# Kernel optimization log

Measured on AMD Instinct MI355X. Metric: run time of the kernel, lower is better.

Reference implementation:

```python
import jax, jax.numpy as jnp
import numpy as np

# dims / hyperparams (match init_kwargs)
B, C, H, W = 1, 48, 160, 160
COUT = 48
RANK = 12
K = 8          # topK neighbors
WS = 32        # window_size
KS = 3         # local conv kernel / local mask size
M = 3          # circ_rows
DELTA = 10.0
LEAK = 0.01


def circ_dense(x, w, m):
    """CircDense: x (N, Cin), w (Cout//m, 1, Cin) -> (N, Cout).
    Equivalent to circular-pad + conv1d in the torch module."""
    cin = x.shape[1]
    xp = jnp.concatenate([x, x[:, : m - 1]], axis=1)            # circular pad to Cin+m-1
    xw = jnp.stack([xp[:, j : j + cin] for j in range(m)], 1)   # (N, m, Cin)
    out = jnp.einsum('njc,ic->nij', xw, w[:, 0, :])             # (N, Cout//m, m)
    return out.reshape(x.shape[0], -1)


def windowed_topk(h, k, ws, ks):
    """knn.windowedTopK: per 32x32 window, K nearest neighbors by feature L2,
    excluding the ks x ks local neighborhood (localMask). Returns (B,K,H,W)
    global flat pixel indices."""
    b, c, hh, ww = h.shape
    nh, nw = hh // ws, ww // ws
    ws2 = ws * ws
    hw = h.reshape(b, c, nh, ws, nw, ws).transpose(0, 2, 4, 3, 5, 1)
    hw = hw.reshape(b, nh, nw, ws2, c)                          # windowed features
    sq = jnp.sum(hw * hw, -1)
    d = sq[..., :, None] + sq[..., None, :] - 2.0 * jnp.einsum('bijnc,bijmc->bijnm', hw, hw)
    r = jnp.arange(ws2) // ws
    cc = jnp.arange(ws2) % ws
    loc = (jnp.abs(r[:, None] - r[None, :]) <= ks // 2) & (jnp.abs(cc[:, None] - cc[None, :]) <= ks // 2)
    d = jnp.where(loc, 1e10, d)                                 # mask local neighborhood
    _, idx = jax.lax.top_k(-d, k)                               # (b,nh,nw,ws2,k) local idx
    wi = jnp.arange(nh)[:, None, None, None]
    wj = jnp.arange(nw)[None, :, None, None]
    g = (wi * ws + idx // ws) * ww + (wj * ws + idx % ws)       # global flat idx
    g = g.reshape(b, nh, nw, ws, ws, k).transpose(0, 5, 1, 3, 2, 4).reshape(b, k, hh, ww)
    return g


def low_rank_ecc(h, edge, W0, b0, WL, WR, Wk, bk):
    b, k, hh, ww = edge.shape
    n = hh * ww
    cin = h.shape[1]
    hf = h.reshape(b, cin, n)
    ef = edge.reshape(b, k, n)
    # gather neighbor (vertex) features: (b, cin, k, n) -> (b, k, n, cin)
    vertex = jax.vmap(lambda hb, eb: hb[:, eb])(hf, ef).transpose(0, 2, 3, 1)
    center = hf.transpose(0, 2, 1)[:, None]                     # (b,1,n,cin)
    label = vertex - center                                     # edge labels
    lt = label.reshape(-1, cin)                                 # (B0, Cin), B0=b*k*n
    vt = vertex.reshape(-1, cin)
    theta = jax.nn.leaky_relu(lt @ W0.T + b0, LEAK)
    tL = circ_dense(theta, WL, M).reshape(-1, COUT, RANK)       # (B0, Cout, rank)
    tR = circ_dense(theta, WR, M).reshape(-1, cin, RANK)        # (B0, Cin, rank)
    kap = theta @ Wk.T + bk                                     # (B0, rank)
    tmp = kap * jnp.einsum('bcr,bc->br', tR, vt)                # thetaR^T @ v, scaled
    out = jnp.einsum('bor,br->bo', tL, tmp)                     # thetaL @ (...)
    gamma = jnp.exp(-jnp.sum(lt * lt, 1, keepdims=True) / DELTA)
    out = (gamma * out).reshape(b, k, n, COUT).mean(1)          # mean over K neighbors
    return out.transpose(0, 2, 1).reshape(b, COUT, hh, ww)


def local_conv(h, w):
    p = KS // 2
    hp = jnp.pad(h, ((0, 0), (0, 0), (p, p), (p, p)), mode='reflect')
    return jax.lax.conv_general_dilated(hp, w, (1, 1), 'VALID',
                                        dimension_numbers=('NCHW', 'OIHW', 'NCHW'))


def setup_inputs() -> dict:
    key = jax.random.key(0)
    ks_ = jax.random.split(key, 9)
    s_in = 1.0 / np.sqrt(C)
    return {
        'h': jax.random.normal(ks_[0], (B, C, H, W), jnp.float32),
        'W0': jax.random.normal(ks_[1], (C, C), jnp.float32) * s_in,
        'b0': jnp.zeros((C,), jnp.float32),
        'WL': jax.random.normal(ks_[2], (RANK * COUT // M, 1, C), jnp.float32) * s_in,
        'WR': jax.random.normal(ks_[3], (RANK * C // M, 1, C), jnp.float32) * s_in,
        'Wk': jax.random.normal(ks_[4], (RANK, C), jnp.float32) * s_in,
        'bk': jnp.zeros((RANK,), jnp.float32),
        'Wconv': jax.random.normal(ks_[5], (COUT, C, KS, KS), jnp.float32) * (1.0 / np.sqrt(C * KS * KS)),
        'bias': jnp.zeros((1, COUT, 1, 1), jnp.float32),
    }


def reference(h, W0, b0, WL, WR, Wk, bk, Wconv, bias):
    edge = windowed_topk(h, K, WS, KS)
    hNL = low_rank_ecc(h, edge, W0, b0, WL, WR, Wk, bk)
    hL = local_conv(h, Wconv)
    return (hNL + hL) / 2.0 + bias
```

## Files before the change

kernel.cpp:

```cpp
#include <hip/hip_runtime.h>

#define CC    48
#define HH    160
#define WWID  160
#define NPIX  25600
#define KK    8

typedef unsigned short u16;
typedef unsigned int u32;
typedef __attribute__((ext_vector_type(8))) short bf16x8;
typedef __attribute__((ext_vector_type(4))) float f32x4;

__device__ __forceinline__ float bf2f(u16 u) {
    return __uint_as_float(((unsigned int)u) << 16);
}
__device__ __forceinline__ u16 f2bf(float f) {
    unsigned int x = __float_as_uint(f);
    return (u16)((x + 0x7FFFu + ((x >> 16) & 1u)) >> 16);
}

#define OFF_B0    0
#define OFF_BK    48
#define OFF_WKT   60
#define OFF_WBH   636
#define OFF_WBL   8828
#define OFF_WLH   17020
#define OFF_WLL   21628
#define OFF_SQP   26236
#define OFF_W0V   51836
#define OFF_VTB   1280636
#define OFF_HHT   3738236
#define OFF_HLT   4557436
#define OFF_PARTK 5376636
#define OFF_UBAR  7015036

__global__ void prep_kernel(const float* W0, const float* b0, const float* WL,
                            const float* WR, const float* Wk, const float* bk,
                            float* ws) {
    float* b0f = ws + OFF_B0;
    float* bkf = ws + OFF_BK;
    float* wkt = ws + OFF_WKT;
    u16*   wbh = (u16*)(ws + OFF_WBH);
    u16*   wbl = (u16*)(ws + OFF_WBL);
    u16*   wlh = (u16*)(ws + OFF_WLH);
    u16*   wll = (u16*)(ws + OFF_WLL);
    int t = blockIdx.x * 256 + threadIdx.x;
    int stride = gridDim.x * 256;
    for (int i = t; i < 16384; i += stride) {
        int col = i >> 6, k = i & 63;
        float v = 0.f;
        if (k < 48) {
            if (col < 192)      v = WR[(4*k + (col & 3))*48 + (col >> 2)];
            else if (col < 240) v = W0[(col - 192)*48 + k];
        }
        u16 hi = f2bf(v);
        wbh[i] = hi;
        wbl[i] = f2bf(v - bf2f(hi));
    }
    for (int i = t; i < 9216; i += stride) {
        int o = i / 192, k = i % 192;
        float v = WL[(4*o + (k & 3))*48 + (k >> 2)];
        u16 hi = f2bf(v);
        wlh[i] = hi;
        wll[i] = f2bf(v - bf2f(hi));
    }
    for (int i = t; i < 576; i += stride) { int c = i / 12, r = i % 12; wkt[i] = Wk[r*48 + c]; }
    for (int i = t; i < 48; i += stride) { b0f[i] = b0[i]; }
    for (int i = t; i < 12; i += stride) { bkf[i] = bk[i]; }
}

__global__ __launch_bounds__(256) void split_kernel(const float* h, float* sqp,
                                                    u16* hht, u16* hlt) {
    int p = blockIdx.x * 256 + threadIdx.x;
    float sq = 0.f;
    u16 hh[64], hl[64];
    #pragma unroll
    for (int c = 0; c < 48; c++) {
        float v = h[c*NPIX + p];
        sq = fmaf(v, v, sq);
        u16 hi = f2bf(v);
        hh[c] = hi;
        hl[c] = f2bf(v - bf2f(hi));
    }
    #pragma unroll
    for (int c = 48; c < 64; c++) { hh[c] = 0; hl[c] = 0; }
    sqp[p] = sq;
    uint4* dh = (uint4*)&hht[(long)p*64];
    uint4* dl = (uint4*)&hlt[(long)p*64];
    const uint4* s1 = (const uint4*)hh;
    const uint4* s2 = (const uint4*)hl;
    #pragma unroll
    for (int i = 0; i < 8; i++) { dh[i] = s1[i]; dl[i] = s2[i]; }
}

__global__ __launch_bounds__(512) void pixvt_mfma(const u16* hht, const u16* hlt,
                                                  const float* ws, float* w0v, u16* vtb) {
    __shared__ __align__(16) char smem[38912];
    u16*   a_hi = (u16*)smem;
    u16*   a_lo = (u16*)(smem + 8192);
    u16*   vt_s = (u16*)smem;
    float* w0_s = (float*)(smem + 25600);

    const u16* wbh = (const u16*)(ws + OFF_WBH);
    const u16* wbl = (const u16*)(ws + OFF_WBL);

    int tid = threadIdx.x;
    int pbase = blockIdx.x * 64;

    {
        int blk = tid >> 6, row = tid & 63;
        int swz = (blk ^ (row & 7)) * 8;
        *(uint4*)&a_hi[row*64 + swz] = *(const uint4*)&hht[(long)(pbase + row)*64 + blk*8];
        *(uint4*)&a_lo[row*64 + swz] = *(const uint4*)&hlt[(long)(pbase + row)*64 + blk*8];
    }
    __syncthreads();

    int w = tid >> 6, lane = tid & 63;
    int lm = lane & 15, lg = lane >> 4;
    int c2a = 2*w, c2b = 2*w + 1;

    f32x4 acc0[4], acc1[4];
    #pragma unroll
    for (int t = 0; t < 4; t++) { acc0[t] = (f32x4){0.f,0.f,0.f,0.f}; acc1[t] = (f32x4){0.f,0.f,0.f,0.f}; }

    #pragma unroll
    for (int s = 0; s < 2; s++) {
        int lblk = 4*s + lg;
        int aswz = (lblk ^ (lm & 7)) * 8;
        bf16x8 ah0 = *(const bf16x8*)&a_hi[( 0 + lm)*64 + aswz];
        bf16x8 ah1 = *(const bf16x8*)&a_hi[(16 + lm)*64 + aswz];
        bf16x8 ah2 = *(const bf16x8*)&a_hi[(32 + lm)*64 + aswz];
        bf16x8 ah3 = *(const bf16x8*)&a_hi[(48 + lm)*64 + aswz];
        bf16x8 al0 = *(const bf16x8*)&a_lo[( 0 + lm)*64 + aswz];
        bf16x8 al1 = *(const bf16x8*)&a_lo[(16 + lm)*64 + aswz];
        bf16x8 al2 = *(const bf16x8*)&a_lo[(32 + lm)*64 + aswz];
        bf16x8 al3 = *(const bf16x8*)&a_lo[(48 + lm)*64 + aswz];
        {
            int col = c2a*16 + lm;
            bf16x8 bh = *(const bf16x8*)&wbh[col*64 + lblk*8];
            bf16x8 bl = *(const bf16x8*)&wbl[col*64 + lblk*8];
            acc0[0] = __builtin_amdgcn_mfma_f32_16x16x32_bf16(ah0, bh, acc0[0], 0, 0, 0);
            acc0[0] = __builtin_amdgcn_mfma_f32_16x16x32_bf16(ah0, bl, acc0[0], 0, 0, 0);
            acc0[0] = __builtin_amdgcn_mfma_f32_16x16x32_bf16(al0, bh, acc0[0], 0, 0, 0);
            acc0[1] = __builtin_amdgcn_mfma_f32_16x16x32_bf16(ah1, bh, acc0[1], 0, 0, 0);
            acc0[1] = __builtin_amdgcn_mfma_f32_16x16x32_bf16(ah1, bl, acc0[1], 0, 0, 0);
            acc0[1] = __builtin_amdgcn_mfma_f32_16x16x32_bf16(al1, bh, acc0[1], 0, 0, 0);
            acc0[2] = __builtin_amdgcn_mfma_f32_16x16x32_bf16(ah2, bh, acc0[2], 0, 0, 0);
            acc0[2] = __builtin_amdgcn_mfma_f32_16x16x32_bf16(ah2, bl, acc0[2], 0, 0, 0);
            acc0[2] = __builtin_amdgcn_mfma_f32_16x16x32_bf16(al2, bh, acc0[2], 0, 0, 0);
            acc0[3] = __builtin_amdgcn_mfma_f32_16x16x32_bf16(ah3, bh, acc0[3], 0, 0, 0);
            acc0[3] = __builtin_amdgcn_mfma_f32_16x16x32_bf16(ah3, bl, acc0[3], 0, 0, 0);
            acc0[3] = __builtin_amdgcn_mfma_f32_16x16x32_bf16(al3, bh, acc0[3], 0, 0, 0);
        }
        if (c2b < 15) {
            int col = c2b*16 + lm;
            bf16x8 bh = *(const bf16x8*)&wbh[col*64 + lblk*8];
            bf16x8 bl = *(const bf16x8*)&wbl[col*64 + lblk*8];
            acc1[0] = __builtin_amdgcn_mfma_f32_16x16x32_bf16(ah0, bh, acc1[0], 0, 0, 0);
            acc1[0] = __builtin_amdgcn_mfma_f32_16x16x32_bf16(ah0, bl, acc1[0], 0, 0, 0);
            acc1[0] = __builtin_amdgcn_mfma_f32_16x16x32_bf16(al0, bh, acc1[0], 0, 0, 0);
            acc1[1] = __builtin_amdgcn_mfma_f32_16x16x32_bf16(ah1, bh, acc1[1], 0, 0, 0);
            acc1[1] = __builtin_amdgcn_mfma_f32_16x16x32_bf16(ah1, bl, acc1[1], 0, 0, 0);
            acc1[1] = __builtin_amdgcn_mfma_f32_16x16x32_bf16(al1, bh, acc1[1], 0, 0, 0);
            acc1[2] = __builtin_amdgcn_mfma_f32_16x16x32_bf16(ah2, bh, acc1[2], 0, 0, 0);
            acc1[2] = __builtin_amdgcn_mfma_f32_16x16x32_bf16(ah2, bl, acc1[2], 0, 0, 0);
            acc1[2] = __builtin_amdgcn_mfma_f32_16x16x32_bf16(al2, bh, acc1[2], 0, 0, 0);
            acc1[3] = __builtin_amdgcn_mfma_f32_16x16x32_bf16(ah3, bh, acc1[3], 0, 0, 0);
            acc1[3] = __builtin_amdgcn_mfma_f32_16x16x32_bf16(ah3, bl, acc1[3], 0, 0, 0);
            acc1[3] = __builtin_amdgcn_mfma_f32_16x16x32_bf16(al3, bh, acc1[3], 0, 0, 0);
        }
    }
    __syncthreads();

    {
        int col = c2a*16 + lm;
        if (c2a < 12) {
            #pragma unroll
            for (int t = 0; t < 4; t++)
                #pragma unroll
                for (int r = 0; r < 4; r++)
                    vt_s[(t*16 + lg*4 + r)*200 + col] = f2bf(acc0[t][r]);
        } else {
            int o = col - 192;
            #pragma unroll
            for (int t = 0; t < 4; t++)
                #pragma unroll
                for (int r = 0; r < 4; r++)
                    w0_s[(t*16 + lg*4 + r)*52 + o] = acc0[t][r];
        }
    }
    if (c2b < 15) {
        int col = c2b*16 + lm;
        if (c2b < 12) {
            #pragma unroll
            for (int t = 0; t < 4; t++)
                #pragma unroll
                for (int r = 0; r < 4; r++)
                    vt_s[(t*16 + lg*4 + r)*200 + col] = f2bf(acc1[t][r]);
        } else {
            int o = col - 192;
            #pragma unroll
            for (int t = 0; t < 4; t++)
                #pragma unroll
                for (int r = 0; r < 4; r++)
                    w0_s[(t*16 + lg*4 + r)*52 + o] = acc1[t][r];
        }
    }
    __syncthreads();

    {
        int px = tid >> 3, c8 = tid & 7;
        #pragma unroll
        for (int j = 0; j < 3; j++) {
            int ch = c8 + 8*j;
            uint4 v = *(const uint4*)&vt_s[px*200 + ch*8];
            *(uint4*)&vtb[(long)(pbase + px)*192 + ch*8] = v;
        }
        float* dst = w0v + (long)(pbase + px)*48 + c8*6;
        const float* src = w0_s + px*52 + c8*6;
        #pragma unroll
        for (int k = 0; k < 3; k++) {
            float2 v2 = *(const float2*)&src[k*2];
            *(float2*)&dst[k*2] = v2;
        }
    }
}

__global__ __launch_bounds__(512, 8) void topk_mfma(const u16* hht, const u16* hlt,
                                                    const float* sqp, u32* partk) {
    __shared__ u16 ca_hi[128*64];
    __shared__ u16 ca_lo[128*64];
    __shared__ float sq_s[128];

    int tid = threadIdx.x;
    int b = (blockIdx.x & 7) * 200 + (blockIdx.x >> 3);
    int chunk = b & 7, pg = (b >> 3) & 7, win = b >> 6;
    int wi = win / 5, wj = win % 5;
    int base = wi*32*WWID + wj*32;

    #pragma unroll
    for (int r = 0; r < 2; r++) {
        int task = r*512 + tid;
        int blk = task >> 7, row = task & 127;
        int swz = (blk ^ (row & 7)) * 8;
        int ml = chunk*128 + row;
        long gp = base + (ml>>5)*WWID + (ml&31);
        *(uint4*)&ca_hi[row*64 + swz] = *(const uint4*)&hht[gp*64 + blk*8];
        *(uint4*)&ca_lo[row*64 + swz] = *(const uint4*)&hlt[gp*64 + blk*8];
    }
    if (tid < 128) {
        int ml = chunk*128 + tid;
        sq_s[tid] = sqp[base + (ml>>5)*WWID + (ml&31)];
    }
    __syncthreads();

    int w = tid >> 6, lane = tid & 63;
    int lm = lane & 15, lg = lane >> 4;

    int nl = pg*128 + w*16 + lm;
    long gpx = base + (nl>>5)*WWID + (nl&31);

    f32x4 acc[8];
    #pragma unroll
    for (int t = 0; t < 8; t++) acc[t] = (f32x4){0.f, 0.f, 0.f, 0.f};

    #pragma unroll
    for (int s = 0; s < 2; s++) {
        int lblk = 4*s + lg;
        int ko = lblk * 8;
        bf16x8 bh = *(const bf16x8*)&hht[gpx*64 + ko];
        bf16x8 bl = *(const bf16x8*)&hlt[gpx*64 + ko];
        #pragma unroll
        for (int t = 0; t < 8; t++) {
            int aoff = (t*16 + lm)*64 + (lblk ^ (lm & 7))*8;
            bf16x8 ah = *(const bf16x8*)&ca_hi[aoff];
            bf16x8 al = *(const bf16x8*)&ca_lo[aoff];
            acc[t] = __builtin_amdgcn_mfma_f32_16x16x32_bf16(ah, bh, acc[t], 0, 0, 0);
            acc[t] = __builtin_amdgcn_mfma_f32_16x16x32_bf16(ah, bl, acc[t], 0, 0, 0);
            acc[t] = __builtin_amdgcn_mfma_f32_16x16x32_bf16(al, bh, acc[t], 0, 0, 0);
        }
    }

    int rn = nl >> 5, cn = nl & 31;
    int rowok[8], colok[8];
    #pragma unroll
    for (int t = 0; t < 8; t++) {
        int rm = chunk*4 + (t >> 1);
        int dr = rn - rm; dr = dr < 0 ? -dr : dr;
        rowok[t] = (dr <= 1);
    }
    #pragma unroll
    for (int j = 0; j < 8; j++) {
        int cm = (j >> 2)*16 + lg*4 + (j & 3);
        int dc = cn - cm; dc = dc < 0 ? -dc : dc;
        colok[j] = (dc <= 1);
    }

    u32 k8[8];
    #pragma unroll
    for (int s = 0; s < 8; s++) k8[s] = 0xFFFFFFFFu;

    #pragma unroll
    for (int t = 0; t < 8; t++) {
        #pragma unroll
        for (int r = 0; r < 4; r++) {
            int cl = t*16 + lg*4 + r;
            int ml = chunk*128 + cl;
            float d = fmaf(-2.0f, acc[t][r], sq_s[cl]);
            u32 u = __float_as_uint(d);
            u32 key = u ^ (0x80000000u | (u32)((int)u >> 31));
            key = (key & 0xFFFFFC00u) | (u32)ml;
            bool bad = rowok[t] && colok[(t & 1)*4 + r];
            key = bad ? 0xFFFFFFFFu : key;
            #pragma unroll
            for (int s = 0; s < 8; s++) {
                u32 lo = min(k8[s], key);
                u32 hi = max(k8[s], key);
                k8[s] = lo; key = hi;
            }
        }
    }

    #pragma unroll
    for (int st = 0; st < 2; st++) {
        int mk = (st == 0) ? 16 : 32;
        u32 o[8];
        #pragma unroll
        for (int s = 0; s < 8; s++) o[s] = (u32)__shfl_xor((int)k8[s], mk, 64);
        u32 c0 = min(k8[0], o[7]);
        u32 c1 = min(k8[1], o[6]);
        u32 c2 = min(k8[2], o[5]);
        u32 c3 = min(k8[3], o[4]);
        u32 c4 = min(k8[4], o[3]);
        u32 c5 = min(k8[5], o[2]);
        u32 c6 = min(k8[6], o[1]);
        u32 c7 = min(k8[7], o[0]);
        u32 a, bb;
        a = min(c0,c4); bb = max(c0,c4); c0 = a; c4 = bb;
        a = min(c1,c5); bb = max(c1,c5); c1 = a; c5 = bb;
        a = min(c2,c6); bb = max(c2,c6); c2 = a; c6 = bb;
        a = min(c3,c7); bb = max(c3,c7); c3 = a; c7 = bb;
        a = min(c0,c2); bb = max(c0,c2); c0 = a; c2 = bb;
        a = min(c1,c3); bb = max(c1,c3); c1 = a; c3 = bb;
        a = min(c4,c6); bb = max(c4,c6); c4 = a; c6 = bb;
        a = min(c5,c7); bb = max(c5,c7); c5 = a; c7 = bb;
        a = min(c0,c1); bb = max(c0,c1); c0 = a; c1 = bb;
        a = min(c2,c3); bb = max(c2,c3); c2 = a; c3 = bb;
        a = min(c4,c5); bb = max(c4,c5); c4 = a; c5 = bb;
        a = min(c6,c7); bb = max(c6,c7); c6 = a; c7 = bb;
        k8[0]=c0; k8[1]=c1; k8[2]=c2; k8[3]=c3; k8[4]=c4; k8[5]=c5; k8[6]=c6; k8[7]=c7;
    }

    {
        int n = base + (nl >> 5)*WWID + (nl & 31);
        u32 v0, v1;
        if      (lg == 0) { v0 = k8[0]; v1 = k8[1]; }
        else if (lg == 1) { v0 = k8[2]; v1 = k8[3]; }
        else if (lg == 2) { v0 = k8[4]; v1 = k8[5]; }
        else              { v0 = k8[6]; v1 = k8[7]; }
        u32* pk = partk + (long)chunk*8*NPIX + (long)(2*lg)*NPIX + n;
        pk[0]    = v0;
        pk[NPIX] = v1;
    }
}

__global__ __launch_bounds__(128, 4) void ecc_kernel(const float* ws, const u32* partk,
                                                     const u16* vtb, u16* ubar) {
    const float* b0f = ws + OFF_B0;
    const float* bkf = ws + OFF_BK;
    const float* wkt = ws + OFF_WKT;
    const float* w0v = ws + OFF_W0V;
    const float* sqp = ws + OFF_SQP;

    __shared__ u16 th_s[128][50];

    int tid = threadIdx.x;
    int sb = (blockIdx.x & 7) * 200 + (blockIdx.x >> 3);
    int pix = tid >> 3, sh = tid & 7;
    int n = sb * 16 + pix;

    u32 k8[8];
    {
        const u32* pk = partk + (long)sh*8*NPIX + n;
        #pragma unroll
        for (int s = 0; s < 8; s++) k8[s] = pk[(long)s*NPIX];
    }
    #pragma unroll
    for (int st = 0; st < 3; st++) {
        int mk = 1 << st;
        u32 o[8];
        #pragma unroll
        for (int s = 0; s < 8; s++) o[s] = (u32)__shfl_xor((int)k8[s], mk, 64);
        u32 c0 = min(k8[0], o[7]);
        u32 c1 = min(k8[1], o[6]);
        u32 c2 = min(k8[2], o[5]);
        u32 c3 = min(k8[3], o[4]);
        u32 c4 = min(k8[4], o[3]);
        u32 c5 = min(k8[5], o[2]);
        u32 c6 = min(k8[6], o[1]);
        u32 c7 = min(k8[7], o[0]);
        u32 a, bb;
        a = min(c0,c4); bb = max(c0,c4); c0 = a; c4 = bb;
        a = min(c1,c5); bb = max(c1,c5); c1 = a; c5 = bb;
        a = min(c2,c6); bb = max(c2,c6); c2 = a; c6 = bb;
        a = min(c3,c7); bb = max(c3,c7); c3 = a; c7 = bb;
        a = min(c0,c2); bb = max(c0,c2); c0 = a; c2 = bb;
        a = min(c1,c3); bb = max(c1,c3); c1 = a; c3 = bb;
        a = min(c4,c6); bb = max(c4,c6); c4 = a; c6 = bb;
        a = min(c5,c7); bb = max(c5,c7); c5 = a; c7 = bb;
        a = min(c0,c1); bb = max(c0,c1); c0 = a; c1 = bb;
        a = min(c2,c3); bb = max(c2,c3); c2 = a; c3 = bb;
        a = min(c4,c5); bb = max(c4,c5); c4 = a; c5 = bb;
        a = min(c6,c7); bb = max(c6,c7); c6 = a; c7 = bb;
        k8[0]=c0; k8[1]=c1; k8[2]=c2; k8[3]=c3; k8[4]=c4; k8[5]=c5; k8[6]=c6; k8[7]=c7;
    }
    u32 key;
    {
        u32 m0 = (sh & 1) ? k8[1] : k8[0];
        u32 m1 = (sh & 1) ? k8[3] : k8[2];
        u32 m2 = (sh & 1) ? k8[5] : k8[4];
        u32 m3 = (sh & 1) ? k8[7] : k8[6];
        u32 n0 = (sh & 2) ? m1 : m0;
        u32 n1 = (sh & 2) ? m3 : m2;
        key = (sh & 4) ? n1 : n0;
    }
    int ml = (int)(key & 1023u);
    u32 uf = key & 0xFFFFFC00u;
    u32 uu = (uf & 0x80000000u) ? (uf ^ 0x80000000u) : ~uf;
    float d = __uint_as_float(uu);
    int y = n / WWID, x = n % WWID;
    int wy = (y >> 5) << 5, wx = (x >> 5) << 5;
    int m = (wy + (ml >> 5)) * WWID + (wx + (ml & 31));
    float gamma = expf(-(d + sqp[n]) * 0.1f);

    float th[48];
    {
        const float4* wm4 = (const float4*)(w0v + (long)m * 48);
        const float4* wn4 = (const float4*)(w0v + (long)n * 48);
        #pragma unroll
        for (int i = 0; i < 12; i++) {
            float4 a = wm4[i];
            float4 b = wn4[i];
            float x0 = a.x - b.x + b0f[4*i+0];
            float x1 = a.y - b.y + b0f[4*i+1];
            float x2 = a.z - b.z + b0f[4*i+2];
            float x3 = a.w - b.w + b0f[4*i+3];
            th[4*i+0] = (x0 >= 0.f) ? x0 : 0.01f * x0;
            th[4*i+1] = (x1 >= 0.f) ? x1 : 0.01f * x1;
            th[4*i+2] = (x2 >= 0.f) ? x2 : 0.01f * x2;
            th[4*i+3] = (x3 >= 0.f) ? x3 : 0.01f * x3;
        }
    }

    #pragma unroll
    for (int i = 0; i < 24; i++) {
        ushort2 pr;
        pr.x = f2bf(th[2*i]);
        pr.y = f2bf(th[2*i+1]);
        *(ushort2*)&th_s[tid][2*i] = pr;
    }

    float kap[12];
    #pragma unroll
    for (int r = 0; r < 12; r++) kap[r] = bkf[r];
    #pragma unroll
    for (int c = 0; c < 48; c++) {
        float t = th[c];
        const float* wkc = wkt + c*12;
        #pragma unroll
        for (int r = 0; r < 12; r++) kap[r] = fmaf(wkc[r], t, kap[r]);
    }

    float sr[12];
    #pragma unroll
    for (int r = 0; r < 12; r++) sr[r] = 0.f;
    const u16* vrow = vtb + (long)m * 192;
    #pragma unroll
    for (int j = 0; j < 24; j++) {
        uint4 vv = *(const uint4*)&vrow[j*8];
        #pragma unroll
        for (int half = 0; half < 2; half++) {
            int cp = 2*j + half;
            u32 w0_ = half ? vv.z : vv.x;
            u32 w1_ = half ? vv.w : vv.y;
            float vx = bf2f((u16)(w0_ & 0xffff));
            float vy = bf2f((u16)(w0_ >> 16));
            float vz = bf2f((u16)(w1_ & 0xffff));
            float vw = bf2f((u16)(w1_ >> 16));
            int i1 = (cp + 1 < 48) ? cp + 1 : cp - 47;
            int i2 = (cp + 2 < 48) ? cp + 2 : cp - 46;
            float t0 = th[cp], t1 = th[i1], t2 = th[i2];
            sr[0] = fmaf(t0, vx, sr[0]); sr[1]  = fmaf(t1, vx, sr[1]);  sr[2]  = fmaf(t2, vx, sr[2]);
            sr[3] = fmaf(t0, vy, sr[3]); sr[4]  = fmaf(t1, vy, sr[4]);  sr[5]  = fmaf(t2, vy, sr[5]);
            sr[6] = fmaf(t0, vz, sr[6]); sr[7]  = fmaf(t1, vz, sr[7]);  sr[8]  = fmaf(t2, vz, sr[8]);
            sr[9] = fmaf(t0, vw, sr[9]); sr[10] = fmaf(t1, vw, sr[10]); sr[11] = fmaf(t2, vw, sr[11]);
        }
    }

    float tmp[12];
    #pragma unroll
    for (int r = 0; r < 12; r++) tmp[r] = kap[r] * sr[r];

    __syncthreads();

    float acc0[6], acc1[6], acc2[6], acc3[6];
    #pragma unroll
    for (int j = 0; j < 6; j++) { acc0[j] = 0.f; acc1[j] = 0.f; acc2[j] = 0.f; acc3[j] = 0.f; }
    #pragma unroll 1
    for (int e = 0; e < 8; e++) {
        int srcl = (tid & 56) + e;
        int row  = (tid & 120) + e;
        float tm[12];
        #pragma unroll
        for (int r = 0; r < 12; r++) tm[r] = __shfl(tmp[r], srcl, 64);
        float ge = __shfl(gamma, srcl, 64);
        #pragma unroll
        for (int j = 0; j < 6; j++) {
            int cp = sh + 8*j;
            int i1 = (cp + 1 < 48) ? cp + 1 : cp - 47;
            int i2 = (cp + 2 < 48) ? cp + 2 : cp - 46;
            float t0 = bf2f(th_s[row][cp]);
            float t1 = bf2f(th_s[row][i1]);
            float t2 = bf2f(th_s[row][i2]);
            float u0 = tm[0]*t0 + tm[1]*t1 + tm[2]*t2;
            float u1 = tm[3]*t0 + tm[4]*t1 + tm[5]*t2;
            float u2 = tm[6]*t0 + tm[7]*t1 + tm[8]*t2;
            float u3 = tm[9]*t0 + tm[10]*t1 + tm[11]*t2;
            acc0[j] = fmaf(ge, u0, acc0[j]);
            acc1[j] = fmaf(ge, u1, acc1[j]);
            acc2[j] = fmaf(ge, u2, acc2[j]);
            acc3[j] = fmaf(ge, u3, acc3[j]);
        }
    }
    u16* ub = ubar + (long)n * 192;
    #pragma unroll
    for (int j = 0; j < 6; j++) {
        int cp = sh + 8*j;
        ushort4 st;
        st.x = f2bf(acc0[j]); st.y = f2bf(acc1[j]);
        st.z = f2bf(acc2[j]); st.w = f2bf(acc3[j]);
        *(ushort4*)&ub[cp*4] = st;
    }
}

__global__ __launch_bounds__(256) void wl_mfma(const float* ws, const u16* ubar, float* outp) {
    __shared__ __align__(16) char smem[25600];
    u16*   a_s = (u16*)smem;
    float* c_s = (float*)smem;

    const u16* wlh = (const u16*)(ws + OFF_WLH);
    const u16* wll = (const u16*)(ws + OFF_WLL);

    int tid = threadIdx.x;
    int pbase = blockIdx.x * 64;

    #pragma unroll
    for (int i = 0; i < 6; i++) {
        int task = i*256 + tid;
        int px = task / 24, ch = task % 24;
        *(uint4*)&a_s[px*200 + ch*8] = *(const uint4*)&ubar[(long)(pbase + px)*192 + ch*8];
    }
    __syncthreads();

    int w = tid >> 6, lane = tid & 63;
    int lm = lane & 15, lg = lane >> 4;

    f32x4 acc[3];
    #pragma unroll
    for (int t = 0; t < 3; t++) acc[t] = (f32x4){0.f, 0.f, 0.f, 0.f};

    #pragma unroll
    for (int ks = 0; ks < 6; ks++) {
        bf16x8 a = *(const bf16x8*)&a_s[(w*16 + lm)*200 + ks*32 + lg*8];
        #pragma unroll
        for (int ct = 0; ct < 3; ct++) {
            int col = ct*16 + lm;
            bf16x8 bh = *(const bf16x8*)&wlh[col*192 + ks*32 + lg*8];
            bf16x8 bl = *(const bf16x8*)&wll[col*192 + ks*32 + lg*8];
            acc[ct] = __builtin_amdgcn_mfma_f32_16x16x32_bf16(a, bh, acc[ct], 0, 0, 0);
            acc[ct] = __builtin_amdgcn_mfma_f32_16x16x32_bf16(a, bl, acc[ct], 0, 0, 0);
        }
    }
    __syncthreads();

    #pragma unroll
    for (int ct = 0; ct < 3; ct++) {
        int o = ct*16 + lm;
        #pragma unroll
        for (int r = 0; r < 4; r++)
            c_s[o*68 + w*16 + lg*4 + r] = 0.0625f * acc[ct][r];
    }
    __syncthreads();

    #pragma unroll
    for (int j = 0; j < 12; j++) {
        int idx = j*256 + tid;
        int o = idx >> 6, px = idx & 63;
        outp[(long)o*NPIX + pbase + px] = c_s[o*68 + px];
    }
}

#define OCH 4
__global__ __launch_bounds__(320) void conv_kernel(const float* h, const float* wc,
                                                   const float* bias, float* outp) {
    int sb = (blockIdx.x & 7) * 120 + (blockIdx.x >> 3);
    int og = sb % 12;
    int yp = sb / 12;
    int t  = threadIdx.x;
    int ty = t / 160;
    int x  = t % 160;
    int y  = yp * 2 + ty;

    int idx9[9];
    #pragma unroll
    for (int dy = 0; dy < 3; dy++) {
        int yy = y + dy - 1;
        yy = yy < 0 ? -yy : (yy >= HH ? 2*HH - 2 - yy : yy);
        #pragma unroll
        for (int dx = 0; dx < 3; dx++) {
            int xx = x + dx - 1;
            xx = xx < 0 ? -xx : (xx >= WWID ? 2*WWID - 2 - xx : xx);
            idx9[dy*3 + dx] = yy * WWID + xx;
        }
    }

    float acc[OCH];
    #pragma unroll
    for (int oi = 0; oi < OCH; oi++) acc[oi] = 0.f;

    const float* wbase = wc + og * OCH * 432;
    for (int c = 0; c < 48; c++) {
        float v[9];
        #pragma unroll
        for (int k = 0; k < 9; k++) v[k] = h[c*NPIX + idx9[k]];
        #pragma unroll
        for (int oi = 0; oi < OCH; oi++) {
            const float* w9 = wbase + oi*432 + c*9;
            float a = acc[oi];
            a = fmaf(v[0], w9[0], a);
            a = fmaf(v[1], w9[1], a);
            a = fmaf(v[2], w9[2], a);
            a = fmaf(v[3], w9[3], a);
            a = fmaf(v[4], w9[4], a);
            a = fmaf(v[5], w9[5], a);
            a = fmaf(v[6], w9[6], a);
            a = fmaf(v[7], w9[7], a);
            a = fmaf(v[8], w9[8], a);
            acc[oi] = a;
        }
    }

    int p = y * WWID + x;
    #pragma unroll
    for (int oi = 0; oi < OCH; oi++) {
        int o = og * OCH + oi;
        outp[o*NPIX + p] = outp[o*NPIX + p] + 0.5f * acc[oi] + bias[o];
    }
}

extern "C" void kernel_launch(void* const* d_in, const int* in_sizes, int n_in,
                              void* d_out, int out_size, void* d_ws, size_t ws_size,
                              hipStream_t stream) {
    const float* h    = (const float*)d_in[0];
    const float* W0   = (const float*)d_in[1];
    const float* b0   = (const float*)d_in[2];
    const float* WL   = (const float*)d_in[3];
    const float* WR   = (const float*)d_in[4];
    const float* Wk   = (const float*)d_in[5];
    const float* bk   = (const float*)d_in[6];
    const float* Wc   = (const float*)d_in[7];
    const float* bias = (const float*)d_in[8];

    float* ws     = (float*)d_ws;
    float* sqp    = ws + OFF_SQP;
    float* w0v    = ws + OFF_W0V;
    u16*   vtb    = (u16*)(ws + OFF_VTB);
    u16*   hht    = (u16*)(ws + OFF_HHT);
    u16*   hlt    = (u16*)(ws + OFF_HLT);
    u32*   partk  = (u32*)(ws + OFF_PARTK);
    u16*   ubar   = (u16*)(ws + OFF_UBAR);
    float* outp   = (float*)d_out;

    prep_kernel<<<dim3(16), dim3(256), 0, stream>>>(W0, b0, WL, WR, Wk, bk, ws);
    split_kernel<<<dim3(100), dim3(256), 0, stream>>>(h, sqp, hht, hlt);
    topk_mfma<<<dim3(1600), dim3(512), 0, stream>>>(hht, hlt, sqp, partk);
    pixvt_mfma<<<dim3(400), dim3(512), 0, stream>>>(hht, hlt, ws, w0v, vtb);
    ecc_kernel<<<dim3(1600), dim3(128), 0, stream>>>(ws, partk, vtb, ubar);
    wl_mfma<<<dim3(400), dim3(256), 0, stream>>>(ws, ubar, outp);
    conv_kernel<<<dim3(960), dim3(320), 0, stream>>>(h, Wc, bias, outp);
}
```

Before: 144.9 us.

## Split ecc_kernel per-edge channel work across thread pairs with 256-thread blocks

Doubles the ecc_kernel block size to 256 threads while keeping 16 pixels per block. Each (pixel, neighbor) pair is now handled by two lanes: each lane does half of the kappa and low-rank dot-product channel loop, and the two halves are combined with xor-1 shuffles. The aggregation phase now uses 16 lanes per pixel, each covering 3 channel groups instead of 6. The aim is more parallelism and lower per-thread register pressure and serial work. The cost is redundant top-k merging, theta and gamma computation in both lanes of a pair, plus extra shuffle traffic.

```diff
diff --git a/kernel.cpp b/kernel.cpp
--- a/kernel.cpp
+++ b/kernel.cpp
@@ -364,8 +364,8 @@
     }
 }
 
-__global__ __launch_bounds__(128, 4) void ecc_kernel(const float* ws, const u32* partk,
-                                                     const u16* vtb, u16* ubar) {
+__global__ __launch_bounds__(256) void ecc_kernel(const float* ws, const u32* partk,
+                                                  const u16* vtb, u16* ubar) {
     const float* b0f = ws + OFF_B0;
     const float* bkf = ws + OFF_BK;
     const float* wkt = ws + OFF_WKT;
@@ -376,12 +376,16 @@
 
     int tid = threadIdx.x;
     int sb = (blockIdx.x & 7) * 200 + (blockIdx.x >> 3);
-    int pix = tid >> 3, sh = tid & 7;
+    int pix = tid >> 4;
     int n = sb * 16 + pix;
+    int lane = tid & 63;
+    int half = tid & 1;
+    int erow = tid >> 1;
+    int ek   = (tid >> 1) & 7;
 
     u32 k8[8];
     {
-        const u32* pk = partk + (long)sh*8*NPIX + n;
+        const u32* pk = partk + (long)(tid & 7)*8*NPIX + n;
         #pragma unroll
         for (int s = 0; s < 8; s++) k8[s] = pk[(long)s*NPIX];
     }
@@ -414,16 +418,18 @@
         a = min(c6,c7); bb = max(c6,c7); c6 = a; c7 = bb;
         k8[0]=c0; k8[1]=c1; k8[2]=c2; k8[3]=c3; k8[4]=c4; k8[5]=c5; k8[6]=c6; k8[7]=c7;
     }
-    u32 key;
+    u32 keyr;
     {
-        u32 m0 = (sh & 1) ? k8[1] : k8[0];
-        u32 m1 = (sh & 1) ? k8[3] : k8[2];
-        u32 m2 = (sh & 1) ? k8[5] : k8[4];
-        u32 m3 = (sh & 1) ? k8[7] : k8[6];
-        u32 n0 = (sh & 2) ? m1 : m0;
-        u32 n1 = (sh & 2) ? m3 : m2;
-        key = (sh & 4) ? n1 : n0;
-    }
+        int sc = tid & 7;
+        u32 m0 = (sc & 1) ? k8[1] : k8[0];
+        u32 m1 = (sc & 1) ? k8[3] : k8[2];
+        u32 m2 = (sc & 1) ? k8[5] : k8[4];
+        u32 m3 = (sc & 1) ? k8[7] : k8[6];
+        u32 n0 = (sc & 2) ? m1 : m0;
+        u32 n1 = (sc & 2) ? m3 : m2;
+        keyr = (sc & 4) ? n1 : n0;
+    }
+    u32 key = (u32)__shfl((int)keyr, (lane & 48) + ek, 64);
     int ml = (int)(key & 1023u);
     u32 uf = key & 0xFFFFFC00u;
     u32 uu = (uf & 0x80000000u) ? (uf ^ 0x80000000u) : ~uf;
@@ -451,38 +457,42 @@
             th[4*i+3] = (x3 >= 0.f) ? x3 : 0.01f * x3;
         }
     }
-
+    #pragma unroll
+    for (int i = 0; i < 12; i++) {
+        int c = half*24 + 2*i;
+        ushort2 pr;
+        pr.x = f2bf(th[c]);
+        pr.y = f2bf(th[c+1]);
+        *(ushort2*)&th_s[erow][c] = pr;
+    }
+
+    float kap[12];
+    #pragma unroll
+    for (int r = 0; r < 12; r++) kap[r] = half ? 0.f : bkf[r];
     #pragma unroll
     for (int i = 0; i < 24; i++) {
-        ushort2 pr;
-        pr.x = f2bf(th[2*i]);
-        pr.y = f2bf(th[2*i+1]);
-        *(ushort2*)&th_s[tid][2*i] = pr;
-    }
-
-    float kap[12];
-    #pragma unroll
-    for (int r = 0; r < 12; r++) kap[r] = bkf[r];
-    #pragma unroll
-    for (int c = 0; c < 48; c++) {
+        int c = half*24 + i;
         float t = th[c];
         const float* wkc = wkt + c*12;
         #pragma unroll
         for (int r = 0; r < 12; r++) kap[r] = fmaf(wkc[r], t, kap[r]);
     }
+    #pragma unroll
+    for (int r = 0; r < 12; r++) kap[r] += __shfl_xor(kap[r], 1, 64);
 
     float sr[12];
     #pragma unroll
     for (int r = 0; r < 12; r++) sr[r] = 0.f;
     const u16* vrow = vtb + (long)m * 192;
     #pragma unroll
-    for (int j = 0; j < 24; j++) {
+    for (int i = 0; i < 12; i++) {
+        int j = half*12 + i;
         uint4 vv = *(const uint4*)&vrow[j*8];
         #pragma unroll
-        for (int half = 0; half < 2; half++) {
-            int cp = 2*j + half;
-            u32 w0_ = half ? vv.z : vv.x;
-            u32 w1_ = half ? vv.w : vv.y;
+        for (int hf = 0; hf < 2; hf++) {
+            int cp = 2*j + hf;
+            u32 w0_ = hf ? vv.z : vv.x;
+            u32 w1_ = hf ? vv.w : vv.y;
             float vx = bf2f((u16)(w0_ & 0xffff));
             float vy = bf2f((u16)(w0_ >> 16));
             float vz = bf2f((u16)(w1_ & 0xffff));
@@ -496,6 +506,8 @@
             sr[9] = fmaf(t0, vw, sr[9]); sr[10] = fmaf(t1, vw, sr[10]); sr[11] = fmaf(t2, vw, sr[11]);
         }
     }
+    #pragma unroll
+    for (int r = 0; r < 12; r++) sr[r] += __shfl_xor(sr[r], 1, 64);
 
     float tmp[12];
     #pragma unroll
@@ -503,20 +515,21 @@
 
     __syncthreads();
 
-    float acc0[6], acc1[6], acc2[6], acc3[6];
-    #pragma unroll
-    for (int j = 0; j < 6; j++) { acc0[j] = 0.f; acc1[j] = 0.f; acc2[j] = 0.f; acc3[j] = 0.f; }
+    int sh16 = tid & 15;
+    float acc0[3], acc1[3], acc2[3], acc3[3];
+    #pragma unroll
+    for (int j = 0; j < 3; j++) { acc0[j] = 0.f; acc1[j] = 0.f; acc2[j] = 0.f; acc3[j] = 0.f; }
     #pragma unroll 1
     for (int e = 0; e < 8; e++) {
-        int srcl = (tid & 56) + e;
-        int row  = (tid & 120) + e;
+        int srcl = (lane & 48) + 2*e;
+        int row  = pix*8 + e;
         float tm[12];
         #pragma unroll
         for (int r = 0; r < 12; r++) tm[r] = __shfl(tmp[r], srcl, 64);
         float ge = __shfl(gamma, srcl, 64);
         #pragma unroll
-        for (int j = 0; j < 6; j++) {
-            int cp = sh + 8*j;
+        for (int j = 0; j < 3; j++) {
+            int cp = sh16 + 16*j;
             int i1 = (cp + 1 < 48) ? cp + 1 : cp - 47;
             int i2 = (cp + 2 < 48) ? cp + 2 : cp - 46;
             float t0 = bf2f(th_s[row][cp]);
@@ -534,8 +547,8 @@
     }
     u16* ub = ubar + (long)n * 192;
     #pragma unroll
-    for (int j = 0; j < 6; j++) {
-        int cp = sh + 8*j;
+    for (int j = 0; j < 3; j++) {
+        int cp = sh16 + 16*j;
         ushort4 st;
         st.x = f2bf(acc0[j]); st.y = f2bf(acc1[j]);
         st.z = f2bf(acc2[j]); st.w = f2bf(acc3[j]);
@@ -685,7 +698,7 @@
     split_kernel<<<dim3(100), dim3(256), 0, stream>>>(h, sqp, hht, hlt);
     topk_mfma<<<dim3(1600), dim3(512), 0, stream>>>(hht, hlt, sqp, partk);
     pixvt_mfma<<<dim3(400), dim3(512), 0, stream>>>(hht, hlt, ws, w0v, vtb);
-    ecc_kernel<<<dim3(1600), dim3(128), 0, stream>>>(ws, partk, vtb, ubar);
+    ecc_kernel<<<dim3(1600), dim3(256), 0, stream>>>(ws, partk, vtb, ubar);
     wl_mfma<<<dim3(400), dim3(256), 0, stream>>>(ws, ubar, outp);
     conv_kernel<<<dim3(960), dim3(320), 0, stream>>>(h, Wc, bias, outp);
 }
```

Result: slower. 187.7 us (+29.6%).
